# Performance work log

Hardware: AMD Instinct MI355X
Metric: run time of the kernel (lower is better)

## Reference

```python
import jax, jax.numpy as jnp
import numpy as np

B, OBS, N, HEADS, SIZE, HID = 8192, 512, 8, 5, 64, 1024
SUM = HEADS * SIZE  # sum(per_robot_dims) = 320
NEG = -1.0e9


def setup_inputs() -> dict:
    key = jax.random.key(0)
    ks = jax.random.split(key, 12)
    init = lambda k, sh, fan: (jax.random.normal(k, sh, jnp.float32) / np.sqrt(fan)).astype(jnp.float32)
    obs = jax.random.normal(ks[0], (B, OBS), jnp.float32)
    actions = jax.random.randint(ks[1], (B, N * HEADS), 0, SIZE)
    masks = jax.random.randint(ks[2], (B, N, HEADS, SIZE), 0, 2).astype(jnp.int32)
    return {
        "obs": obs,
        "actions": actions,
        "masks": masks,
        "W1": init(ks[3], (OBS, HID), OBS), "b1": jnp.zeros((HID,), jnp.float32),
        "W2": init(ks[4], (HID, HID), HID), "b2": jnp.zeros((HID,), jnp.float32),
        "headsW": init(ks[5], (N, HID, SUM), HID), "headsb": jnp.zeros((N, SUM), jnp.float32),
        "Wc1": init(ks[6], (HID, HID // 2), HID), "bc1": jnp.zeros((HID // 2,), jnp.float32),
        "Wc2": init(ks[7], (HID // 2, 1), HID // 2), "bc2": jnp.zeros((1,), jnp.float32),
    }


def reference(obs, actions, masks, W1, b1, W2, b2, headsW, headsb, Wc1, bc1, Wc2, bc2):
    # Shared encoder: two Linear+ReLU layers.
    h = jax.nn.relu(obs @ W1 + b1)
    h = jax.nn.relu(h @ W2 + b2)  # [B, HID]
    # Per-robot heads, batched into one einsum: [B, N, SUM]
    logits = jnp.einsum('bh,nhs->bns', h, headsW) + headsb
    seg = logits.reshape(B, N, HEADS, SIZE)
    # Masked softmax: invalid entries set to -1e9 (matches seg[~mask] = -1e9).
    seg = jnp.where(masks.astype(bool), seg, NEG)
    logp = jax.nn.log_softmax(seg, axis=-1)          # [B, N, HEADS, SIZE]
    probs = jnp.exp(logp)
    acts = actions.reshape(B, N, HEADS)
    lp_terms = jnp.take_along_axis(logp, acts[..., None], axis=-1)[..., 0]
    ent_terms = -jnp.sum(probs * logp, axis=-1)
    # Out-of-range action -> log-prob -1000 and no entropy contribution.
    valid = acts < SIZE
    logps = jnp.where(valid, lp_terms, -1000.0).sum(axis=(1, 2))
    entropy = jnp.where(valid, ent_terms, 0.0).sum(axis=(1, 2))
    # Critic value head.
    values = (jax.nn.relu(h @ Wc1 + bc1) @ Wc2 + bc2)[..., 0]
    return logps, entropy, values
```

## Files before the change

kernel.cpp:

```cpp
#include <hip/hip_runtime.h>
#include <hip/hip_bf16.h>
#include <stdint.h>


typedef __bf16 v8bf __attribute__((ext_vector_type(8)));
typedef float  v4f  __attribute__((ext_vector_type(4)));

__device__ __forceinline__ void load_lds16(const void* g, void* l) {
  auto gp = (const __attribute__((address_space(1))) char*)(uintptr_t)g;
  auto lp = (__attribute__((address_space(3))) char*)(uintptr_t)l;
  __builtin_amdgcn_global_load_lds(gp, lp, 16, 0, 0);
}

#define BARRIER __builtin_amdgcn_s_barrier()
#define SCHEDB  __builtin_amdgcn_sched_barrier(0)
#define WAIT_LGKM0 do { asm volatile("s_waitcnt lgkmcnt(0)" ::: "memory"); SCHEDB; } while (0)
#define WAIT_LGKM8 do { asm volatile("s_waitcnt lgkmcnt(8)" ::: "memory"); SCHEDB; } while (0)
#define WAIT_VM8   do { asm volatile("s_waitcnt vmcnt(8)" ::: "memory"); SCHEDB; } while (0)
#define WAIT_VM0   do { asm volatile("s_waitcnt vmcnt(0)" ::: "memory"); SCHEDB; } while (0)


__global__ void convert_obs(const float4* __restrict__ in, int4* __restrict__ out, int n8) {
  const int i = blockIdx.x * blockDim.x + threadIdx.x;
  if (i >= n8) return;
  const float4 x = in[i * 2], y = in[i * 2 + 1];
  union { __hip_bfloat16 h[8]; int4 v; } u;
  u.h[0] = __float2bfloat16(x.x);
  u.h[1] = __float2bfloat16(x.y);
  u.h[2] = __float2bfloat16(x.z);
  u.h[3] = __float2bfloat16(x.w);
  u.h[4] = __float2bfloat16(y.x);
  u.h[5] = __float2bfloat16(y.y);
  u.h[6] = __float2bfloat16(y.z);
  u.h[7] = __float2bfloat16(y.w);
  out[i] = u.v;
}

__global__ void build_bias(const float* __restrict__ headsb, const float* __restrict__ bc1,
                           float* __restrict__ biasc) {
  const int i = blockIdx.x * blockDim.x + threadIdx.x;
  if (i < 2560) biasc[i] = headsb[i];
  else if (i < 3072) biasc[i] = bc1[i - 2560];
}

__global__ void transpose_to_bf16(const float* __restrict__ in, __hip_bfloat16* __restrict__ out,
                                  int R, int C) {
  __shared__ float t[32][33];
  const int bx = blockIdx.x * 32, by = blockIdx.y * 32;
  in  += (size_t)blockIdx.z * R * C;
  out += (size_t)blockIdx.z * R * C;
  const int x = threadIdx.x, y = threadIdx.y;
#pragma unroll
  for (int i = 0; i < 32; i += 8)
    t[y + i][x] = in[(size_t)(by + y + i) * C + bx + x];
  __syncthreads();
#pragma unroll
  for (int i = 0; i < 32; i += 8)
    out[(size_t)(bx + y + i) * R + by + x] = __float2bfloat16(t[x][y + i]);
}


__device__ __forceinline__ void decode_chunk(int o, int& r, int& cb) {
  const int L = o ^ (((o >> 9) & 1) << 5);
  r  = ((L >> 10) << 4) | ((L >> 6) & 15);
  cb = ((L >> 4) & 3) << 4;
}

__global__ __launch_bounds__(256, 2)
void gemm_db(const __hip_bfloat16* __restrict__ A,
             const __hip_bfloat16* __restrict__ Bt,
             const float* __restrict__ bias,
             __hip_bfloat16* __restrict__ C,
             int N, int K, int relu_from, int gx) {
  __shared__ char smem[65536];

  const int tid  = threadIdx.x;
  const int lane = tid & 63;
  const int wave = tid >> 6;
  const int wr = wave >> 1, wc = wave & 1;
  const int lr = lane & 15, ls = lane >> 4;

  const int nwg = gridDim.x;
  const int q8 = nwg >> 3;
  const int id = (blockIdx.x & 7) * q8 + (blockIdx.x >> 3);
  const int bx = id % gx, by = id / gx;
  const int m0 = by * 128, n0 = bx * 128;

  int r0, c0, r1, c1;
  decode_chunk(tid * 16, r0, c0);
  decode_chunk(tid * 16 + 4096, r1, c1);

  const size_t K2 = (size_t)K * 2;
  const char* pA0 = (const char*)A  + (size_t)(m0 + r0) * K2 + c0;
  const char* pA1 = (const char*)A  + (size_t)(m0 + r1) * K2 + c1;
  const char* pB0 = (const char*)Bt + (size_t)(n0 + r0) * K2 + c0;
  const char* pB1 = (const char*)Bt + (size_t)(n0 + r1) * K2 + c1;

  char* const s0 = smem + (tid << 4);

  auto stage = [&](int buf) {
    char* d = s0 + (buf << 15);
    load_lds16(pA0,      d);
    load_lds16(pA1,      d + 4096);
    load_lds16(pA0 + 64, d + 8192);
    load_lds16(pA1 + 64, d + 12288);
    load_lds16(pB0,      d + 16384);
    load_lds16(pB1,      d + 20480);
    load_lds16(pB0 + 64, d + 24576);
    load_lds16(pB1 + 64, d + 28672);
    pA0 += 128; pA1 += 128; pB0 += 128; pB1 += 128;
  };

  const int laneOff = lr * 64 + ((ls * 16) ^ ((lr & 8) << 2));

  v4f acc[4][4] = {};

  auto tile = [&](int buf, bool doStage, auto gate) {
    const char* aB = smem + (buf << 15) + wr * 4096 + laneOff;
    const char* bB = smem + (buf << 15) + 16384 + wc * 4096 + laneOff;
    v8bf a0[4], b0[4], a1[4], b1[4];
#pragma unroll
    for (int m = 0; m < 4; ++m) a0[m] = *(const v8bf*)(aB + m * 1024);
#pragma unroll
    for (int n = 0; n < 4; ++n) b0[n] = *(const v8bf*)(bB + n * 1024);
#pragma unroll
    for (int m = 0; m < 4; ++m) a1[m] = *(const v8bf*)(aB + 8192 + m * 1024);
#pragma unroll
    for (int n = 0; n < 4; ++n) b1[n] = *(const v8bf*)(bB + 8192 + n * 1024);
    WAIT_LGKM8;
    __builtin_amdgcn_s_setprio(1);
#pragma unroll
    for (int m = 0; m < 4; ++m)
#pragma unroll
      for (int n = 0; n < 4; ++n)
        acc[m][n] = __builtin_amdgcn_mfma_f32_16x16x32_bf16(a0[m], b0[n], acc[m][n], 0, 0, 0);
    __builtin_amdgcn_s_setprio(0); SCHEDB;
    WAIT_LGKM0;
    BARRIER;
    if (doStage) stage(buf);
    __builtin_amdgcn_s_setprio(1);
#pragma unroll
    for (int m = 0; m < 4; ++m)
#pragma unroll
      for (int n = 0; n < 4; ++n)
        acc[m][n] = __builtin_amdgcn_mfma_f32_16x16x32_bf16(a1[m], b1[n], acc[m][n], 0, 0, 0);
    __builtin_amdgcn_s_setprio(0); SCHEDB;
    gate();
    BARRIER;
  };

  stage(0);
  stage(1);
  WAIT_VM8;
  BARRIER; SCHEDB;

  const int NT = K >> 6;
  int t = 0;
  for (; t < NT - 2; ++t)
    tile(t & 1, true, [] { WAIT_VM8; });
  tile(t & 1, false, [] { WAIT_VM0; }); ++t;
  tile(t & 1, false, [] {});

  const int colb = n0 + wc * 64 + lr;
  const int rowb = m0 + wr * 64 + ls * 4;
#pragma unroll
  for (int n = 0; n < 4; ++n) {
    const int col = colb + n * 16;
    const float bv = bias[col];
    const bool rl = (col >= relu_from);
#pragma unroll
    for (int m = 0; m < 4; ++m) {
      const int rbase = rowb + m * 16;
#pragma unroll
      for (int j = 0; j < 4; ++j) {
        float v = acc[m][n][j] + bv;
        if (rl) v = fmaxf(v, 0.0f);
        C[(size_t)(rbase + j) * N + col] = __float2bfloat16(v);
      }
    }
  }
}


__global__ __launch_bounds__(256)
void finalize_kernel(const __hip_bfloat16* __restrict__ out3,
                     const int* __restrict__ masks,
                     const int* __restrict__ actions,
                     const float* __restrict__ Wc2,
                     const float* __restrict__ bc2,
                     float* __restrict__ out) {
  const int lane = threadIdx.x & 63;
  const int r = blockIdx.x * 4 + (threadIdx.x >> 6);
  const __hip_bfloat16* row = out3 + (size_t)r * 3072;
  const int* mrow = masks + (size_t)r * 2560;
  const int* arow = actions + r * 40;

  const int g = lane >> 3;

  float lp_sum = 0.f, ent_sum = 0.f;

#pragma unroll
  for (int p = 0; p < 5; ++p) {
    const int base = p * 512 + lane * 8;
    union { int4 q; __hip_bfloat16 h[8]; } u;
    u.q = *(const int4*)(row + base);
    const int4 ma = *(const int4*)(mrow + base);
    const int4 mb = *(const int4*)(mrow + base + 4);

    float v[8];
    v[0] = ma.x ? __bfloat162float(u.h[0]) : -1.0e9f;
    v[1] = ma.y ? __bfloat162float(u.h[1]) : -1.0e9f;
    v[2] = ma.z ? __bfloat162float(u.h[2]) : -1.0e9f;
    v[3] = ma.w ? __bfloat162float(u.h[3]) : -1.0e9f;
    v[4] = mb.x ? __bfloat162float(u.h[4]) : -1.0e9f;
    v[5] = mb.y ? __bfloat162float(u.h[5]) : -1.0e9f;
    v[6] = mb.z ? __bfloat162float(u.h[6]) : -1.0e9f;
    v[7] = mb.w ? __bfloat162float(u.h[7]) : -1.0e9f;

    float mx = fmaxf(fmaxf(fmaxf(v[0], v[1]), fmaxf(v[2], v[3])),
                     fmaxf(fmaxf(v[4], v[5]), fmaxf(v[6], v[7])));
#pragma unroll
    for (int o = 1; o < 8; o <<= 1) mx = fmaxf(mx, __shfl_xor(mx, o));

    float s = 0.f, sv = 0.f;
#pragma unroll
    for (int j = 0; j < 8; ++j) {
      const float e = __expf(v[j] - mx);
      s += e;
      sv += e * v[j];
    }
#pragma unroll
    for (int o = 1; o < 8; o <<= 1) { s += __shfl_xor(s, o); sv += __shfl_xor(sv, o); }

    const float logZ = __logf(s) + mx;

    const int act = arow[p * 8 + g];
    float va_loc = v[0];
#pragma unroll
    for (int j = 1; j < 8; ++j) va_loc = ((act & 7) == j) ? v[j] : va_loc;
    const float va = __shfl(va_loc, (lane & 56) | ((act >> 3) & 7));

    if ((unsigned)act < 64u) {
      lp_sum += va - logZ;
      ent_sum += logZ - sv / s;
    } else {
      lp_sum += -1000.0f;
    }
  }

#pragma unroll
  for (int o = 8; o < 64; o <<= 1) {
    lp_sum += __shfl_xor(lp_sum, o);
    ent_sum += __shfl_xor(ent_sum, o);
  }

  union { int4 q; __hip_bfloat16 h[8]; } c;
  c.q = *(const int4*)(row + 2560 + lane * 8);
  const float4 w0 = *(const float4*)(Wc2 + lane * 8);
  const float4 w1 = *(const float4*)(Wc2 + lane * 8 + 4);
  float acc = __bfloat162float(c.h[0]) * w0.x + __bfloat162float(c.h[1]) * w0.y +
              __bfloat162float(c.h[2]) * w0.z + __bfloat162float(c.h[3]) * w0.w +
              __bfloat162float(c.h[4]) * w1.x + __bfloat162float(c.h[5]) * w1.y +
              __bfloat162float(c.h[6]) * w1.z + __bfloat162float(c.h[7]) * w1.w;
#pragma unroll
  for (int o = 32; o > 0; o >>= 1) acc += __shfl_xor(acc, o);

  if (lane == 0) {
    out[r]         = lp_sum;
    out[8192 + r]  = ent_sum;
    out[16384 + r] = acc + bc2[0];
  }
}


extern "C" void kernel_launch(void* const* d_in, const int* in_sizes, int n_in,
                              void* d_out, int out_size, void* d_ws, size_t ws_size,
                              hipStream_t stream) {
  const float* obs    = (const float*)d_in[0];
  const int*   actions= (const int*)d_in[1];
  const int*   masks  = (const int*)d_in[2];
  const float* W1     = (const float*)d_in[3];
  const float* b1     = (const float*)d_in[4];
  const float* W2     = (const float*)d_in[5];
  const float* b2     = (const float*)d_in[6];
  const float* headsW = (const float*)d_in[7];
  const float* headsb = (const float*)d_in[8];
  const float* Wc1    = (const float*)d_in[9];
  const float* bc1    = (const float*)d_in[10];
  const float* Wc2    = (const float*)d_in[11];
  const float* bc2    = (const float*)d_in[12];
  float* out = (float*)d_out;

  char* ws = (char*)d_ws;
  __hip_bfloat16* obsB  = (__hip_bfloat16*)(ws);
  __hip_bfloat16* W1t   = (__hip_bfloat16*)(ws + 8388608);
  __hip_bfloat16* W2t   = (__hip_bfloat16*)(ws + 9437184);
  __hip_bfloat16* Wbigt = (__hip_bfloat16*)(ws + 11534336);
  float*          biasc = (float*)(ws + 17825792);
  __hip_bfloat16* h1    = (__hip_bfloat16*)(ws + 17838080);
  __hip_bfloat16* h2    = (__hip_bfloat16*)(ws + 34615296);
  __hip_bfloat16* out3  = (__hip_bfloat16*)(ws + 51392512);

  convert_obs<<<2048, 256, 0, stream>>>((const float4*)obs, (int4*)obsB, 524288);
  build_bias<<<12, 256, 0, stream>>>(headsb, bc1, biasc);
  transpose_to_bf16<<<dim3(32, 16, 1), dim3(32, 8), 0, stream>>>(W1, W1t, 512, 1024);
  transpose_to_bf16<<<dim3(32, 32, 1), dim3(32, 8), 0, stream>>>(W2, W2t, 1024, 1024);
  transpose_to_bf16<<<dim3(10, 32, 8), dim3(32, 8), 0, stream>>>(headsW, Wbigt, 1024, 320);
  transpose_to_bf16<<<dim3(16, 32, 1), dim3(32, 8), 0, stream>>>(Wc1, Wbigt + 2560 * 1024, 1024, 512);

  gemm_db<<<dim3(512), 256, 0, stream>>>(obsB, W1t, b1, h1, 1024, 512, 0, 8);
  gemm_db<<<dim3(512), 256, 0, stream>>>(h1, W2t, b2, h2, 1024, 1024, 0, 8);
  gemm_db<<<dim3(1536), 256, 0, stream>>>(h2, Wbigt, biasc, out3, 3072, 1024, 2560, 24);

  finalize_kernel<<<2048, 256, 0, stream>>>(out3, masks, actions, Wc2, bc2, out);
}
```

Baseline: 137.9 us.

## Add 256x256-tile 8-wave GEMM with interleaved staging for head projection

Adds a new GEMM kernel that uses 256x256 output tiles with 512 threads (8 waves, each computing a 128x64 sub-tile) and 128KB double-buffered LDS. It uses it for the largest GEMM, the fused heads plus critic projection (N=3072). Global-to-LDS staging is interleaved between MFMA quadrants, and the MFMA sections are wrapped in barriers and s_setprio. The larger tiles are meant to raise arithmetic intensity and cut redundant A/B loads. In exchange the grid drops to 384 blocks, which may lower occupancy and leave tail imbalance across CUs.

Measured after the change: 147.9 us. 1.07x slower.

```diff
diff --git a/kernel.cpp b/kernel.cpp
--- a/kernel.cpp
+++ b/kernel.cpp
@@ -66,6 +66,7 @@
   cb = ((L >> 4) & 3) << 4;
 }
 
+
 __global__ __launch_bounds__(256, 2)
 void gemm_db(const __hip_bfloat16* __restrict__ A,
              const __hip_bfloat16* __restrict__ Bt,
@@ -170,6 +171,139 @@
     const bool rl = (col >= relu_from);
 #pragma unroll
     for (int m = 0; m < 4; ++m) {
+      const int rbase = rowb + m * 16;
+#pragma unroll
+      for (int j = 0; j < 4; ++j) {
+        float v = acc[m][n][j] + bv;
+        if (rl) v = fmaxf(v, 0.0f);
+        C[(size_t)(rbase + j) * N + col] = __float2bfloat16(v);
+      }
+    }
+  }
+}
+
+
+template<int M0, int N0>
+__device__ __forceinline__ void q16(v4f (&acc)[8][4], const v8bf (&aF)[4][2],
+                                    const v8bf (&bF)[4][2]) {
+#pragma unroll
+  for (int m = 0; m < 4; ++m)
+#pragma unroll
+    for (int n = 0; n < 2; ++n)
+#pragma unroll
+      for (int ks = 0; ks < 2; ++ks)
+        acc[M0 + m][N0 + n] = __builtin_amdgcn_mfma_f32_16x16x32_bf16(
+            aF[m][ks], bF[N0 + n][ks], acc[M0 + m][N0 + n], 0, 0, 0);
+}
+
+__global__ __launch_bounds__(512, 2)
+void gemm_256(const __hip_bfloat16* __restrict__ A,
+              const __hip_bfloat16* __restrict__ Bt,
+              const float* __restrict__ bias,
+              __hip_bfloat16* __restrict__ C,
+              int N, int K, int relu_from, int gx) {
+  __shared__ char smem[131072];
+
+  const int tid  = threadIdx.x;
+  const int lane = tid & 63;
+  const int wave = tid >> 6;
+  const int wr = wave >> 2;
+  const int wc = wave & 3;
+  const int lr = lane & 15, ls = lane >> 4;
+
+  const int nwg = gridDim.x;
+  const int q8 = nwg >> 3;
+  const int id = (blockIdx.x & 7) * q8 + (blockIdx.x >> 3);
+  const int bx = id % gx, by = id / gx;
+  const int m0 = by * 256, n0 = bx * 256;
+
+  int r0, c0;
+  decode_chunk(tid * 16, r0, c0);
+
+  const size_t K2 = (size_t)K * 2;
+  const char* pA0 = (const char*)A  + (size_t)(m0 +       r0) * K2 + c0;
+  const char* pA1 = (const char*)A  + (size_t)(m0 + 128 + r0) * K2 + c0;
+  const char* pB0 = (const char*)Bt + (size_t)(n0 +       r0) * K2 + c0;
+  const char* pB1 = (const char*)Bt + (size_t)(n0 + 128 + r0) * K2 + c0;
+
+  char* const s0 = smem + (tid << 4);
+
+  auto stA = [&](int db) {
+    char* d = s0 + (db << 16);
+    load_lds16(pA0,      d);
+    load_lds16(pA0 + 64, d + 8192);
+    load_lds16(pA1,      d + 16384);
+    load_lds16(pA1 + 64, d + 24576);
+    pA0 += 128; pA1 += 128;
+  };
+  auto stB = [&](int db) {
+    char* d = s0 + (db << 16) + 32768;
+    load_lds16(pB0,      d);
+    load_lds16(pB0 + 64, d + 8192);
+    load_lds16(pB1,      d + 16384);
+    load_lds16(pB1 + 64, d + 24576);
+    pB0 += 128; pB1 += 128;
+  };
+
+  const int laneOff = lr * 64 + ((ls * 16) ^ ((lr & 8) << 2));
+
+  v4f acc[8][4] = {};
+
+  auto ktile = [&](int db, bool doStage, int gateMode) {
+    const char* aB = smem + (db << 16) + wr * 16384 + laneOff;
+    const char* bB = smem + (db << 16) + 32768 + (wc >> 1) * 16384 + (wc & 1) * 4096 + laneOff;
+    v8bf aF[4][2], bF[4][2];
+#pragma unroll
+    for (int m = 0; m < 4; ++m)
+#pragma unroll
+      for (int ks = 0; ks < 2; ++ks) aF[m][ks] = *(const v8bf*)(aB + ks * 8192 + m * 1024);
+#pragma unroll
+    for (int n = 0; n < 4; ++n)
+#pragma unroll
+      for (int ks = 0; ks < 2; ++ks) bF[n][ks] = *(const v8bf*)(bB + ks * 8192 + n * 1024);
+    BARRIER; WAIT_LGKM0;
+    __builtin_amdgcn_s_setprio(1); q16<0, 0>(acc, aF, bF); __builtin_amdgcn_s_setprio(0); SCHEDB;
+    BARRIER;
+    __builtin_amdgcn_s_setprio(1); q16<0, 2>(acc, aF, bF); __builtin_amdgcn_s_setprio(0); SCHEDB;
+    BARRIER;
+#pragma unroll
+    for (int m = 0; m < 4; ++m)
+#pragma unroll
+      for (int ks = 0; ks < 2; ++ks) aF[m][ks] = *(const v8bf*)(aB + ks * 8192 + (4 + m) * 1024);
+    if (doStage) stB(db);
+    BARRIER; WAIT_LGKM0;
+    __builtin_amdgcn_s_setprio(1); q16<4, 2>(acc, aF, bF); __builtin_amdgcn_s_setprio(0); SCHEDB;
+    BARRIER;
+    if (doStage) stA(db);
+    BARRIER;
+    __builtin_amdgcn_s_setprio(1); q16<4, 0>(acc, aF, bF); __builtin_amdgcn_s_setprio(0); SCHEDB;
+    if (gateMode == 0) { WAIT_VM8; }
+    else if (gateMode == 1) { WAIT_VM0; }
+    BARRIER;
+  };
+
+  stA(0); stB(0);
+  stA(1); stB(1);
+  WAIT_VM8;
+  BARRIER; SCHEDB;
+
+  const int NP = K >> 7;
+  for (int i = 0; i < NP - 1; ++i) {
+    ktile(0, true, 0);
+    ktile(1, true, 0);
+  }
+  ktile(0, false, 1);
+  ktile(1, false, 2);
+
+  const int colb = n0 + wc * 64 + lr;
+  const int rowb = m0 + wr * 128 + ls * 4;
+#pragma unroll
+  for (int n = 0; n < 4; ++n) {
+    const int col = colb + n * 16;
+    const float bv = bias[col];
+    const bool rl = (col >= relu_from);
+#pragma unroll
+    for (int m = 0; m < 8; ++m) {
       const int rbase = rowb + m * 16;
 #pragma unroll
       for (int j = 0; j < 4; ++j) {
@@ -310,7 +444,7 @@
 
   gemm_db<<<dim3(512), 256, 0, stream>>>(obsB, W1t, b1, h1, 1024, 512, 0, 8);
   gemm_db<<<dim3(512), 256, 0, stream>>>(h1, W2t, b2, h2, 1024, 1024, 0, 8);
-  gemm_db<<<dim3(1536), 256, 0, stream>>>(h2, Wbigt, biasc, out3, 3072, 1024, 2560, 24);
+  gemm_256<<<dim3(384), 512, 0, stream>>>(h2, Wbigt, biasc, out3, 3072, 1024, 2560, 12);
 
   finalize_kernel<<<2048, 256, 0, stream>>>(out3, masks, actions, Wc2, bc2, out);
 }
```

## Fuse masked log-softmax into head GEMM epilogue and merge prep kernels

Applied to the files above, without the earlier changes.

Merges the six preprocessing launches (obs conversion, bias build, four weight transposes) into one prep kernel dispatched by block index. Adds a dedicated head GEMM whose epilogue applies the mask, computes per-segment log-softmax, picks the action log-prob and computes entropy directly from fp32 accumulators. It writes only small per-segment partials plus the critic hidden activations. This removes the bf16 logits round trip and leaves a light finalize kernel, at the cost of scattered per-lane mask loads in the epilogue and extra shuffle work inside the GEMM. Logits are also no longer rounded to bf16 before the softmax.

Result: slower. 142.1 us (+3.0%).

```diff
diff --git a/kernel.cpp b/kernel.cpp
--- a/kernel.cpp
+++ b/kernel.cpp
@@ -20,43 +20,50 @@
 #define WAIT_VM0   do { asm volatile("s_waitcnt vmcnt(0)" ::: "memory"); SCHEDB; } while (0)
 
 
-__global__ void convert_obs(const float4* __restrict__ in, int4* __restrict__ out, int n8) {
-  const int i = blockIdx.x * blockDim.x + threadIdx.x;
-  if (i >= n8) return;
-  const float4 x = in[i * 2], y = in[i * 2 + 1];
-  union { __hip_bfloat16 h[8]; int4 v; } u;
-  u.h[0] = __float2bfloat16(x.x);
-  u.h[1] = __float2bfloat16(x.y);
-  u.h[2] = __float2bfloat16(x.z);
-  u.h[3] = __float2bfloat16(x.w);
-  u.h[4] = __float2bfloat16(y.x);
-  u.h[5] = __float2bfloat16(y.y);
-  u.h[6] = __float2bfloat16(y.z);
-  u.h[7] = __float2bfloat16(y.w);
-  out[i] = u.v;
-}
-
-__global__ void build_bias(const float* __restrict__ headsb, const float* __restrict__ bc1,
-                           float* __restrict__ biasc) {
-  const int i = blockIdx.x * blockDim.x + threadIdx.x;
-  if (i < 2560) biasc[i] = headsb[i];
-  else if (i < 3072) biasc[i] = bc1[i - 2560];
-}
-
-__global__ void transpose_to_bf16(const float* __restrict__ in, __hip_bfloat16* __restrict__ out,
-                                  int R, int C) {
-  __shared__ float t[32][33];
-  const int bx = blockIdx.x * 32, by = blockIdx.y * 32;
-  in  += (size_t)blockIdx.z * R * C;
-  out += (size_t)blockIdx.z * R * C;
-  const int x = threadIdx.x, y = threadIdx.y;
-#pragma unroll
-  for (int i = 0; i < 32; i += 8)
-    t[y + i][x] = in[(size_t)(by + y + i) * C + bx + x];
-  __syncthreads();
-#pragma unroll
-  for (int i = 0; i < 32; i += 8)
-    out[(size_t)(bx + y + i) * R + by + x] = __float2bfloat16(t[x][y + i]);
+__global__ __launch_bounds__(256)
+void prep_kernel(const float* __restrict__ obs,
+                 const float* __restrict__ W1, const float* __restrict__ W2,
+                 const float* __restrict__ headsW, const float* __restrict__ Wc1,
+                 const float* __restrict__ headsb, const float* __restrict__ bc1,
+                 int4* __restrict__ obsB,
+                 __hip_bfloat16* __restrict__ W1t, __hip_bfloat16* __restrict__ W2t,
+                 __hip_bfloat16* __restrict__ Wbigt, float* __restrict__ biasc) {
+  const int b = blockIdx.x;
+  const int tid = threadIdx.x;
+  if (b < 4608) {
+    const float* in; __hip_bfloat16* outp; int R, C, bxx, byy;
+    if (b < 512)       { in = W1;  outp = W1t; R = 512;  C = 1024; bxx = b % 32; byy = b / 32; }
+    else if (b < 1536) { int i = b - 512;  in = W2;  outp = W2t; R = 1024; C = 1024; bxx = i % 32; byy = i / 32; }
+    else if (b < 4096) { int i = b - 1536; int bz = i / 320; i %= 320;
+                         in = headsW + (size_t)bz * 1024 * 320;
+                         outp = Wbigt + (size_t)bz * 320 * 1024;
+                         R = 1024; C = 320; bxx = i % 10; byy = i / 10; }
+    else               { int i = b - 4096; in = Wc1; outp = Wbigt + 2560 * 1024;
+                         R = 1024; C = 512; bxx = i % 16; byy = i / 16; }
+    __shared__ float t[32][33];
+    const int x = tid & 31, y = tid >> 5;
+    const int bx0 = bxx * 32, by0 = byy * 32;
+#pragma unroll
+    for (int i = 0; i < 32; i += 8)
+      t[y + i][x] = in[(size_t)(by0 + y + i) * C + bx0 + x];
+    __syncthreads();
+#pragma unroll
+    for (int i = 0; i < 32; i += 8)
+      outp[(size_t)(bx0 + y + i) * R + by0 + x] = __float2bfloat16(t[x][y + i]);
+  } else if (b < 6656) {
+    const int i = (b - 4608) * 256 + tid;
+    const float4 x = ((const float4*)obs)[i * 2], y = ((const float4*)obs)[i * 2 + 1];
+    union { __hip_bfloat16 h[8]; int4 v; } u;
+    u.h[0] = __float2bfloat16(x.x); u.h[1] = __float2bfloat16(x.y);
+    u.h[2] = __float2bfloat16(x.z); u.h[3] = __float2bfloat16(x.w);
+    u.h[4] = __float2bfloat16(y.x); u.h[5] = __float2bfloat16(y.y);
+    u.h[6] = __float2bfloat16(y.z); u.h[7] = __float2bfloat16(y.w);
+    obsB[i] = u.v;
+  } else {
+    const int i = (b - 6656) * 256 + tid;
+    if (i < 2560) biasc[i] = headsb[i];
+    else if (i < 3072) biasc[i] = bc1[i - 2560];
+  }
 }
 
 
@@ -65,6 +72,7 @@
   r  = ((L >> 10) << 4) | ((L >> 6) & 15);
   cb = ((L >> 4) & 3) << 4;
 }
+
 
 __global__ __launch_bounds__(256, 2)
 void gemm_db(const __hip_bfloat16* __restrict__ A,
@@ -182,80 +190,185 @@
 }
 
 
+__global__ __launch_bounds__(256, 2)
+void gemm_fused(const __hip_bfloat16* __restrict__ A,
+                const __hip_bfloat16* __restrict__ Bt,
+                const float* __restrict__ bias,
+                const int* __restrict__ masks,
+                const int* __restrict__ actions,
+                float2* __restrict__ partials,
+                __hip_bfloat16* __restrict__ critic,
+                int K) {
+  __shared__ char smem[65536];
+
+  const int tid  = threadIdx.x;
+  const int lane = tid & 63;
+  const int wave = tid >> 6;
+  const int wr = wave >> 1, wc = wave & 1;
+  const int lr = lane & 15, ls = lane >> 4;
+
+  const int nwg = gridDim.x;
+  const int q8 = nwg >> 3;
+  const int id = (blockIdx.x & 7) * q8 + (blockIdx.x >> 3);
+  const int bx = id % 24, by = id / 24;
+  const int m0 = by * 128, n0 = bx * 128;
+
+  int r0, c0, r1, c1;
+  decode_chunk(tid * 16, r0, c0);
+  decode_chunk(tid * 16 + 4096, r1, c1);
+
+  const size_t K2 = (size_t)K * 2;
+  const char* pA0 = (const char*)A  + (size_t)(m0 + r0) * K2 + c0;
+  const char* pA1 = (const char*)A  + (size_t)(m0 + r1) * K2 + c1;
+  const char* pB0 = (const char*)Bt + (size_t)(n0 + r0) * K2 + c0;
+  const char* pB1 = (const char*)Bt + (size_t)(n0 + r1) * K2 + c1;
+
+  char* const s0 = smem + (tid << 4);
+
+  auto stage = [&](int buf) {
+    char* d = s0 + (buf << 15);
+    load_lds16(pA0,      d);
+    load_lds16(pA1,      d + 4096);
+    load_lds16(pA0 + 64, d + 8192);
+    load_lds16(pA1 + 64, d + 12288);
+    load_lds16(pB0,      d + 16384);
+    load_lds16(pB1,      d + 20480);
+    load_lds16(pB0 + 64, d + 24576);
+    load_lds16(pB1 + 64, d + 28672);
+    pA0 += 128; pA1 += 128; pB0 += 128; pB1 += 128;
+  };
+
+  const int laneOff = lr * 64 + ((ls * 16) ^ ((lr & 8) << 2));
+
+  v4f acc[4][4] = {};
+
+  auto tile = [&](int buf, bool doStage, auto gate) {
+    const char* aB = smem + (buf << 15) + wr * 4096 + laneOff;
+    const char* bB = smem + (buf << 15) + 16384 + wc * 4096 + laneOff;
+    v8bf a0[4], b0[4], a1[4], b1[4];
+#pragma unroll
+    for (int m = 0; m < 4; ++m) a0[m] = *(const v8bf*)(aB + m * 1024);
+#pragma unroll
+    for (int n = 0; n < 4; ++n) b0[n] = *(const v8bf*)(bB + n * 1024);
+#pragma unroll
+    for (int m = 0; m < 4; ++m) a1[m] = *(const v8bf*)(aB + 8192 + m * 1024);
+#pragma unroll
+    for (int n = 0; n < 4; ++n) b1[n] = *(const v8bf*)(bB + 8192 + n * 1024);
+    WAIT_LGKM8;
+    __builtin_amdgcn_s_setprio(1);
+#pragma unroll
+    for (int m = 0; m < 4; ++m)
+#pragma unroll
+      for (int n = 0; n < 4; ++n)
+        acc[m][n] = __builtin_amdgcn_mfma_f32_16x16x32_bf16(a0[m], b0[n], acc[m][n], 0, 0, 0);
+    __builtin_amdgcn_s_setprio(0); SCHEDB;
+    WAIT_LGKM0;
+    BARRIER;
+    if (doStage) stage(buf);
+    __builtin_amdgcn_s_setprio(1);
+#pragma unroll
+    for (int m = 0; m < 4; ++m)
+#pragma unroll
+      for (int n = 0; n < 4; ++n)
+        acc[m][n] = __builtin_amdgcn_mfma_f32_16x16x32_bf16(a1[m], b1[n], acc[m][n], 0, 0, 0);
+    __builtin_amdgcn_s_setprio(0); SCHEDB;
+    gate();
+    BARRIER;
+  };
+
+  stage(0);
+  stage(1);
+  WAIT_VM8;
+  BARRIER; SCHEDB;
+
+  const int NT = K >> 6;
+  int t = 0;
+  for (; t < NT - 2; ++t)
+    tile(t & 1, true, [] { WAIT_VM8; });
+  tile(t & 1, false, [] { WAIT_VM0; }); ++t;
+  tile(t & 1, false, [] {});
+
+  const int rowb = m0 + wr * 64 + ls * 4;
+
+  if (bx < 20) {
+    const int seg = bx * 2 + wc;
+    float bv[4];
+#pragma unroll
+    for (int n = 0; n < 4; ++n) bv[n] = bias[n0 + wc * 64 + n * 16 + lr];
+#pragma unroll
+    for (int m = 0; m < 4; ++m) {
+#pragma unroll
+      for (int j = 0; j < 4; ++j) {
+        const int row = rowb + m * 16 + j;
+        const int* mrow = masks + (size_t)row * 2560 + seg * 64 + lr;
+        float v[4];
+#pragma unroll
+        for (int n = 0; n < 4; ++n) {
+          const int mk = mrow[n * 16];
+          v[n] = mk ? (acc[m][n][j] + bv[n]) : -1.0e9f;
+        }
+        float mx = fmaxf(fmaxf(v[0], v[1]), fmaxf(v[2], v[3]));
+#pragma unroll
+        for (int o = 1; o < 16; o <<= 1) mx = fmaxf(mx, __shfl_xor(mx, o));
+        float s = 0.f, sv = 0.f;
+#pragma unroll
+        for (int n = 0; n < 4; ++n) {
+          const float e = __expf(v[n] - mx);
+          s += e; sv += e * v[n];
+        }
+#pragma unroll
+        for (int o = 1; o < 16; o <<= 1) { s += __shfl_xor(s, o); sv += __shfl_xor(sv, o); }
+        const float logZ = __logf(s) + mx;
+        const int act = actions[row * 40 + seg];
+        float va_loc = v[0];
+        va_loc = (((act >> 4) & 3) == 1) ? v[1] : va_loc;
+        va_loc = (((act >> 4) & 3) == 2) ? v[2] : va_loc;
+        va_loc = (((act >> 4) & 3) == 3) ? v[3] : va_loc;
+        const float va = __shfl(va_loc, (lane & 48) | (act & 15));
+        float lp, ent;
+        if ((unsigned)act < 64u) { lp = va - logZ; ent = logZ - sv / s; }
+        else                     { lp = -1000.0f;  ent = 0.0f; }
+        if (lr == 0) partials[row * 40 + seg] = make_float2(lp, ent);
+      }
+    }
+  } else {
+    const int cb = (bx - 20) * 128 + wc * 64;
+#pragma unroll
+    for (int n = 0; n < 4; ++n) {
+      const int col = cb + n * 16 + lr;
+      const float bvv = bias[2560 + col];
+#pragma unroll
+      for (int m = 0; m < 4; ++m) {
+        const int rbase = rowb + m * 16;
+#pragma unroll
+        for (int j = 0; j < 4; ++j)
+          critic[(size_t)(rbase + j) * 512 + col] =
+              __float2bfloat16(fmaxf(acc[m][n][j] + bvv, 0.0f));
+      }
+    }
+  }
+}
+
+
 __global__ __launch_bounds__(256)
-void finalize_kernel(const __hip_bfloat16* __restrict__ out3,
-                     const int* __restrict__ masks,
-                     const int* __restrict__ actions,
-                     const float* __restrict__ Wc2,
-                     const float* __restrict__ bc2,
-                     float* __restrict__ out) {
+void finalize3(const float2* __restrict__ partials,
+               const __hip_bfloat16* __restrict__ critic,
+               const float* __restrict__ Wc2,
+               const float* __restrict__ bc2,
+               float* __restrict__ out) {
   const int lane = threadIdx.x & 63;
   const int r = blockIdx.x * 4 + (threadIdx.x >> 6);
-  const __hip_bfloat16* row = out3 + (size_t)r * 3072;
-  const int* mrow = masks + (size_t)r * 2560;
-  const int* arow = actions + r * 40;
-
-  const int g = lane >> 3;
-
-  float lp_sum = 0.f, ent_sum = 0.f;
-
-#pragma unroll
-  for (int p = 0; p < 5; ++p) {
-    const int base = p * 512 + lane * 8;
-    union { int4 q; __hip_bfloat16 h[8]; } u;
-    u.q = *(const int4*)(row + base);
-    const int4 ma = *(const int4*)(mrow + base);
-    const int4 mb = *(const int4*)(mrow + base + 4);
-
-    float v[8];
-    v[0] = ma.x ? __bfloat162float(u.h[0]) : -1.0e9f;
-    v[1] = ma.y ? __bfloat162float(u.h[1]) : -1.0e9f;
-    v[2] = ma.z ? __bfloat162float(u.h[2]) : -1.0e9f;
-    v[3] = ma.w ? __bfloat162float(u.h[3]) : -1.0e9f;
-    v[4] = mb.x ? __bfloat162float(u.h[4]) : -1.0e9f;
-    v[5] = mb.y ? __bfloat162float(u.h[5]) : -1.0e9f;
-    v[6] = mb.z ? __bfloat162float(u.h[6]) : -1.0e9f;
-    v[7] = mb.w ? __bfloat162float(u.h[7]) : -1.0e9f;
-
-    float mx = fmaxf(fmaxf(fmaxf(v[0], v[1]), fmaxf(v[2], v[3])),
-                     fmaxf(fmaxf(v[4], v[5]), fmaxf(v[6], v[7])));
-#pragma unroll
-    for (int o = 1; o < 8; o <<= 1) mx = fmaxf(mx, __shfl_xor(mx, o));
-
-    float s = 0.f, sv = 0.f;
-#pragma unroll
-    for (int j = 0; j < 8; ++j) {
-      const float e = __expf(v[j] - mx);
-      s += e;
-      sv += e * v[j];
-    }
-#pragma unroll
-    for (int o = 1; o < 8; o <<= 1) { s += __shfl_xor(s, o); sv += __shfl_xor(sv, o); }
-
-    const float logZ = __logf(s) + mx;
-
-    const int act = arow[p * 8 + g];
-    float va_loc = v[0];
-#pragma unroll
-    for (int j = 1; j < 8; ++j) va_loc = ((act & 7) == j) ? v[j] : va_loc;
-    const float va = __shfl(va_loc, (lane & 56) | ((act >> 3) & 7));
-
-    if ((unsigned)act < 64u) {
-      lp_sum += va - logZ;
-      ent_sum += logZ - sv / s;
-    } else {
-      lp_sum += -1000.0f;
-    }
+
+  float lp = 0.f, ent = 0.f;
+  if (lane < 40) {
+    const float2 t = partials[r * 40 + lane];
+    lp = t.x; ent = t.y;
   }
-
-#pragma unroll
-  for (int o = 8; o < 64; o <<= 1) {
-    lp_sum += __shfl_xor(lp_sum, o);
-    ent_sum += __shfl_xor(ent_sum, o);
-  }
+#pragma unroll
+  for (int o = 32; o > 0; o >>= 1) { lp += __shfl_xor(lp, o); ent += __shfl_xor(ent, o); }
 
   union { int4 q; __hip_bfloat16 h[8]; } c;
-  c.q = *(const int4*)(row + 2560 + lane * 8);
+  c.q = *(const int4*)(critic + (size_t)r * 512 + lane * 8);
   const float4 w0 = *(const float4*)(Wc2 + lane * 8);
   const float4 w1 = *(const float4*)(Wc2 + lane * 8 + 4);
   float acc = __bfloat162float(c.h[0]) * w0.x + __bfloat162float(c.h[1]) * w0.y +
@@ -266,8 +379,8 @@
   for (int o = 32; o > 0; o >>= 1) acc += __shfl_xor(acc, o);
 
   if (lane == 0) {
-    out[r]         = lp_sum;
-    out[8192 + r]  = ent_sum;
+    out[r]         = lp;
+    out[8192 + r]  = ent;
     out[16384 + r] = acc + bc2[0];
   }
 }
@@ -299,18 +412,17 @@
   float*          biasc = (float*)(ws + 17825792);
   __hip_bfloat16* h1    = (__hip_bfloat16*)(ws + 17838080);
   __hip_bfloat16* h2    = (__hip_bfloat16*)(ws + 34615296);
-  __hip_bfloat16* out3  = (__hip_bfloat16*)(ws + 51392512);
-
-  convert_obs<<<2048, 256, 0, stream>>>((const float4*)obs, (int4*)obsB, 524288);
-  build_bias<<<12, 256, 0, stream>>>(headsb, bc1, biasc);
-  transpose_to_bf16<<<dim3(32, 16, 1), dim3(32, 8), 0, stream>>>(W1, W1t, 512, 1024);
-  transpose_to_bf16<<<dim3(32, 32, 1), dim3(32, 8), 0, stream>>>(W2, W2t, 1024, 1024);
-  transpose_to_bf16<<<dim3(10, 32, 8), dim3(32, 8), 0, stream>>>(headsW, Wbigt, 1024, 320);
-  transpose_to_bf16<<<dim3(16, 32, 1), dim3(32, 8), 0, stream>>>(Wc1, Wbigt + 2560 * 1024, 1024, 512);
+  float2*      partials = (float2*)(ws + 51392512);
+  __hip_bfloat16* critic= (__hip_bfloat16*)(ws + 54013952);
+
+  prep_kernel<<<6668, 256, 0, stream>>>(obs, W1, W2, headsW, Wc1, headsb, bc1,
+                                        (int4*)obsB, W1t, W2t, Wbigt, biasc);
 
   gemm_db<<<dim3(512), 256, 0, stream>>>(obsB, W1t, b1, h1, 1024, 512, 0, 8);
   gemm_db<<<dim3(512), 256, 0, stream>>>(h1, W2t, b2, h2, 1024, 1024, 0, 8);
-  gemm_db<<<dim3(1536), 256, 0, stream>>>(h2, Wbigt, biasc, out3, 3072, 1024, 2560, 24);
-
-  finalize_kernel<<<2048, 256, 0, stream>>>(out3, masks, actions, Wc2, bc2, out);
-}
+
+  gemm_fused<<<dim3(1536), 256, 0, stream>>>(h2, Wbigt, biasc, masks, actions,
+                                             partials, critic, 1024);
+
+  finalize3<<<2048, 256, 0, stream>>>(partials, critic, Wc2, bc2, out);
+}
```
